# Kernel tuning notes

Measured on AMD Instinct MI355X. Metric: run time of the kernel, lower is better.

The kernel has to match this reference:

```python
import jax, jax.numpy as jnp
import numpy as np

B, I, H, R = 8192, 512, 1024, 64  # batch, input_size, hidden_size, rank (w_rank == u_ranks[-1])


def setup_inputs() -> dict:
    key = jax.random.key(0)
    ks = jax.random.split(key, 11)
    f = jax.random.normal
    return {
        "x": f(ks[0], (B, I), jnp.float32),
        "h": f(ks[1], (B, H), jnp.float32),
        "c": f(ks[2], (B, H), jnp.float32),
        "u_x": 0.1 * f(ks[3], (I, R), jnp.float32),
        "u_h": 0.1 * f(ks[4], (H, R), jnp.float32),
        "v_x": 0.1 * f(ks[5], (4 * H, R), jnp.float32),
        "v_h": 0.1 * f(ks[6], (4 * H, R), jnp.float32),
        "b_x": 0.1 * f(ks[7], (4 * H,), jnp.float32),
        "b_h": 0.1 * f(ks[8], (4 * H,), jnp.float32),
        "dia_x": 0.1 * f(ks[9], (1, I), jnp.float32),
        "dia_h": 0.1 * f(ks[10], (1, H), jnp.float32),
    }


def reference(x, h, c, u_x, u_h, v_x, v_h, b_x, b_h, dia_x, dia_h):
    Bn = x.shape[0]
    # diagonal (vector-multiplication) terms; vm_x padded to hidden size (H >= I)
    vm_x = jnp.pad(dia_x * x, ((0, 0), (0, H - I)))          # [B, H]
    vm_h = dia_h * h                                          # [B, H]
    # low-rank projections: [B,R] @ [R,4H]
    lowered_x = (x @ u_x) @ v_x.T                             # [B, 4H]
    lowered_h = (h @ u_h) @ v_h.T                             # [B, 4H]
    # vectorized form of the 4-gate refinement loop
    v_x4 = v_x.reshape(4, H, R)
    v_h4 = v_h.reshape(4, H, R)
    coef_x = jnp.sum(u_x[None] * v_x4[:, :I, :], axis=-1)    # [4, I]
    coef_h = jnp.sum(u_h[None] * v_h4, axis=-1)              # [4, H]
    ref_x = jnp.pad(x[:, None, :] * coef_x[None], ((0, 0), (0, 0), (0, H - I))).reshape(Bn, 4 * H)
    ref_h = (h[:, None, :] * coef_h[None]).reshape(Bn, 4 * H)
    gx = lowered_x - ref_x + b_x
    gh = lowered_h - ref_h + b_h
    xi, xf, xo, xn = jnp.split(gx, 4, axis=1)
    hi, hf, ho, hn = jnp.split(gh, 4, axis=1)
    z = vm_x + vm_h
    inputgate = jax.nn.sigmoid(xi + hi + z)
    forgetgate = jax.nn.sigmoid(xf + hf + z)
    outputgate = jax.nn.sigmoid(xo + ho + z)
    newgate = jnp.tanh(xn + hn + z)
    c_next = forgetgate * c + inputgate * newgate
    h_next = outputgate * jnp.tanh(c_next)
    return h_next, c_next
```

## Files before the change

### kernel.cpp

```cpp
#include <hip/hip_runtime.h>
#include <hip/hip_bf16.h>

#define B_ 8192
#define I_ 512
#define H_ 1024
#define R_ 64

typedef __bf16 bf16x8 __attribute__((ext_vector_type(8)));
typedef short  s16x8  __attribute__((ext_vector_type(8)));
typedef float  f32x4  __attribute__((ext_vector_type(4)));

static __device__ __forceinline__ short f2bf(float f) {
    union { float f; unsigned u; } v; v.f = f;
    unsigned r = v.u + 0x7fffu + ((v.u >> 16) & 1u);
    return (short)(r >> 16);
}

static __device__ __forceinline__ float sigmoidf_(float v) {
    return 1.f / (1.f + __expf(-v));
}
static __device__ __forceinline__ float tanhf_(float v) {
    return 2.f / (1.f + __expf(-2.f * v)) - 1.f;
}

__global__ __launch_bounds__(256) void prep_kernel(
    const float* __restrict__ u_x, const float* __restrict__ u_h,
    const float* __restrict__ v_x, const float* __restrict__ v_h,
    short* __restrict__ uxT, short* __restrict__ uhT, short* __restrict__ Vc,
    float* __restrict__ coef_x, float* __restrict__ coef_h)
{
    int t = blockIdx.x * 256 + threadIdx.x;
    if (t < 64 * 512) {
        int k = t >> 6, r = t & 63;
        uxT[r * 512 + k] = f2bf(u_x[t]);
        return;
    }
    t -= 64 * 512;
    if (t < 64 * 1024) {
        int k = t >> 6, r = t & 63;
        uhT[r * 1024 + k] = f2bf(u_h[t]);
        return;
    }
    t -= 64 * 1024;
    if (t < 4096 * 128) {
        int n = t >> 7, q = t & 127;
        Vc[t] = f2bf(q < 64 ? v_x[n * 64 + q] : v_h[n * 64 + (q - 64)]);
        return;
    }
    t -= 4096 * 128;
    if (t < 4 * 512) {
        int g = t / 512, j = t % 512;
        const float4* up = (const float4*)(u_x + (size_t)j * 64);
        const float4* vp = (const float4*)(v_x + (size_t)(g * H_ + j) * 64);
        float s = 0.f;
#pragma unroll
        for (int r = 0; r < 16; ++r) {
            float4 a = up[r], b = vp[r];
            s += a.x * b.x + a.y * b.y + a.z * b.z + a.w * b.w;
        }
        coef_x[t] = s;
        return;
    }
    t -= 4 * 512;
    if (t < 4 * 1024) {
        int g = t >> 10, j = t & 1023;
        const float4* up = (const float4*)(u_h + (size_t)j * 64);
        const float4* vp = (const float4*)(v_h + (size_t)(g * H_ + j) * 64);
        float s = 0.f;
#pragma unroll
        for (int r = 0; r < 16; ++r) {
            float4 a = up[r], b = vp[r];
            s += a.x * b.x + a.y * b.y + a.z * b.z + a.w * b.w;
        }
        coef_h[t] = s;
        return;
    }
}

__global__ __launch_bounds__(1024) void stage1_kernel(
    const float* __restrict__ x, const float* __restrict__ h,
    const short* __restrict__ uxT, const short* __restrict__ uhT,
    short* __restrict__ P)
{
    __shared__ short At[64 * 136];
    const int w = threadIdx.x >> 6, lane = threadIdx.x & 63;
    const int quad = lane >> 4, lr = lane & 15;
    const int mt = w >> 2;
    const int n0 = (w & 3) * 16;

    const float* X; const short* UT; int K, co;
    if (blockIdx.y == 0) { X = x; UT = uxT; K = I_; co = 0; }
    else                 { X = h; UT = uhT; K = H_; co = 64; }

    const int b0 = blockIdx.x * 64;
    const int srow = threadIdx.x >> 4;
    const int scol = (threadIdx.x & 15) * 8;

    f32x4 acc = {};
    const short* bp = UT + (size_t)(n0 + lr) * K + quad * 8;
    const short* arow = At + (mt * 16 + lr) * 136 + quad * 8;

    for (int k0 = 0; k0 < K; k0 += 128) {
        const float* src = X + (size_t)(b0 + srow) * K + k0 + scol;
        float4 v0 = ((const float4*)src)[0];
        float4 v1 = ((const float4*)src)[1];
        s16x8 p;
        p[0] = f2bf(v0.x); p[1] = f2bf(v0.y); p[2] = f2bf(v0.z); p[3] = f2bf(v0.w);
        p[4] = f2bf(v1.x); p[5] = f2bf(v1.y); p[6] = f2bf(v1.z); p[7] = f2bf(v1.w);
        __syncthreads();
        *(s16x8*)(At + srow * 136 + scol) = p;
        __syncthreads();
#pragma unroll
        for (int ks = 0; ks < 4; ++ks) {
            bf16x8 bfrag = *(const bf16x8*)(bp + k0 + ks * 32);
            bf16x8 afrag = *(const bf16x8*)(arow + ks * 32);
            acc = __builtin_amdgcn_mfma_f32_16x16x32_bf16(afrag, bfrag, acc, 0, 0, 0);
        }
    }

#pragma unroll
    for (int r = 0; r < 4; ++r)
        P[(size_t)(b0 + mt * 16 + quad * 4 + r) * 128 + co + n0 + lr] = f2bf(acc[r]);
}

__global__ __launch_bounds__(256) void stage2_kernel(
    const short* __restrict__ P, const short* __restrict__ Vc,
    const float* __restrict__ x, const float* __restrict__ h,
    const float* __restrict__ c,
    const float* __restrict__ coef_x, const float* __restrict__ coef_h,
    const float* __restrict__ b_x, const float* __restrict__ b_h,
    const float* __restrict__ dia_x, const float* __restrict__ dia_h,
    float* __restrict__ out)
{
    __shared__ short Bt[4 * 16 * 136];
    const int w = threadIdx.x >> 6, lane = threadIdx.x & 63;
    const int quad = lane >> 4, lr = lane & 15;
    const int b0 = blockIdx.x * 256 + w * 64;
    const int j0 = blockIdx.y * 16;
    const int j = j0 + lr;
    const bool jx = (j < I_);

    {
        const int row = threadIdx.x >> 2;
        const int g = row >> 4, jj = row & 15;
        const int col = (threadIdx.x & 3) * 32;
        const short* src = Vc + (size_t)(g * H_ + j0 + jj) * 128 + col;
        short* dst = Bt + (g * 16 + jj) * 136 + col;
        *(s16x8*)(dst)      = *(const s16x8*)(src);
        *(s16x8*)(dst + 8)  = *(const s16x8*)(src + 8);
        *(s16x8*)(dst + 16) = *(const s16x8*)(src + 16);
        *(s16x8*)(dst + 24) = *(const s16x8*)(src + 24);
    }

    const float dx = jx ? dia_x[j] : 0.f;
    const float dh = dia_h[j];
    float cx[4], ch[4], bsum[4];
#pragma unroll
    for (int g = 0; g < 4; ++g) {
        cx[g]   = jx ? coef_x[g * I_ + j] : 0.f;
        ch[g]   = coef_h[g * H_ + j];
        bsum[g] = b_x[g * H_ + j] + b_h[g * H_ + j];
    }
    __syncthreads();

    for (int mt = 0; mt < 4; ++mt) {
        const int r0 = b0 + mt * 16;

        float xv[4], hv[4], cv[4];
#pragma unroll
        for (int r = 0; r < 4; ++r) {
            const int brow = r0 + quad * 4 + r;
            cv[r] = c[(size_t)brow * H_ + j];
            hv[r] = h[(size_t)brow * H_ + j];
            xv[r] = jx ? x[(size_t)brow * I_ + j] : 0.f;
        }

        f32x4 acc[4] = {};
#pragma unroll
        for (int ks = 0; ks < 4; ++ks) {
            bf16x8 a = *(const bf16x8*)(P + (size_t)(r0 + lr) * 128 + ks * 32 + quad * 8);
#pragma unroll
            for (int g = 0; g < 4; ++g) {
                bf16x8 b = *(const bf16x8*)(Bt + (g * 16 + lr) * 136 + ks * 32 + quad * 8);
                acc[g] = __builtin_amdgcn_mfma_f32_16x16x32_bf16(a, b, acc[g], 0, 0, 0);
            }
        }

#pragma unroll
        for (int r = 0; r < 4; ++r) {
            const int brow = r0 + quad * 4 + r;
            const float xe = xv[r], he = hv[r];
            const float z  = dx * xe + dh * he;

            const float g0 = acc[0][r] - xe * cx[0] - he * ch[0] + bsum[0] + z;
            const float g1 = acc[1][r] - xe * cx[1] - he * ch[1] + bsum[1] + z;
            const float g2 = acc[2][r] - xe * cx[2] - he * ch[2] + bsum[2] + z;
            const float g3 = acc[3][r] - xe * cx[3] - he * ch[3] + bsum[3] + z;

            const float ig = sigmoidf_(g0);
            const float fg = sigmoidf_(g1);
            const float og = sigmoidf_(g2);
            const float ng = tanhf_(g3);

            const float cn = fg * cv[r] + ig * ng;
            const float hn = og * tanhf_(cn);

            out[(size_t)brow * H_ + j] = hn;
            out[(size_t)B_ * H_ + (size_t)brow * H_ + j] = cn;
        }
    }
}

extern "C" void kernel_launch(void* const* d_in, const int* in_sizes, int n_in,
                              void* d_out, int out_size, void* d_ws, size_t ws_size,
                              hipStream_t stream) {
    const float* x     = (const float*)d_in[0];
    const float* h     = (const float*)d_in[1];
    const float* c     = (const float*)d_in[2];
    const float* u_x   = (const float*)d_in[3];
    const float* u_h   = (const float*)d_in[4];
    const float* v_x   = (const float*)d_in[5];
    const float* v_h   = (const float*)d_in[6];
    const float* b_x   = (const float*)d_in[7];
    const float* b_h   = (const float*)d_in[8];
    const float* dia_x = (const float*)d_in[9];
    const float* dia_h = (const float*)d_in[10];
    float* out = (float*)d_out;

    char* ws = (char*)d_ws;
    short* P      = (short*)(ws);
    short* uxT    = (short*)(ws + 2097152);
    short* uhT    = (short*)(ws + 2097152 + 65536);
    short* Vc     = (short*)(ws + 2097152 + 65536 + 131072);
    float* coef_x = (float*)(ws + 2097152 + 65536 + 131072 + 1048576);
    float* coef_h = (float*)(ws + 2097152 + 65536 + 131072 + 1048576 + 8192);

    prep_kernel<<<2456, 256, 0, stream>>>(u_x, u_h, v_x, v_h, uxT, uhT, Vc, coef_x, coef_h);
    stage1_kernel<<<dim3(128, 2), 1024, 0, stream>>>(x, h, uxT, uhT, P);
    stage2_kernel<<<dim3(32, 64), 256, 0, stream>>>(P, Vc, x, h, c,
                                                    coef_x, coef_h, b_x, b_h,
                                                    dia_x, dia_h, out);
}
```

Baseline: 200.6 us.

## Fuse low-rank projection and gate stages into one kernel with LDS-resident P

Merges stage1 and stage2 into a single main_kernel: each block projects 64 batch rows of x and h onto rank space, keeps the bf16 P tile in shared memory, and then computes a 512-wide hidden slice of the gate outputs while prefetching the next column's x/h/c. This removes the global round-trip for P and one launch, and the prep coef computation becomes wave-level shuffle reductions. The trade-off is that the grid shrinks to 256 blocks and each block redoes the projection for both hidden halves, so it does duplicate GEMM work and has less parallelism. V is now read directly from global memory rather than staged in LDS.

```diff
diff --git a/kernel.cpp b/kernel.cpp
--- a/kernel.cpp
+++ b/kernel.cpp
@@ -5,6 +5,7 @@
 #define I_ 512
 #define H_ 1024
 #define R_ 64
+#define PITCH 136
 
 typedef __bf16 bf16x8 __attribute__((ext_vector_type(8)));
 typedef short  s16x8  __attribute__((ext_vector_type(8)));
@@ -15,7 +16,6 @@
     unsigned r = v.u + 0x7fffu + ((v.u >> 16) & 1u);
     return (short)(r >> 16);
 }
-
 static __device__ __forceinline__ float sigmoidf_(float v) {
     return 1.f / (1.f + __expf(-v));
 }
@@ -48,147 +48,157 @@
         return;
     }
     t -= 4096 * 128;
-    if (t < 4 * 512) {
-        int g = t / 512, j = t % 512;
-        const float4* up = (const float4*)(u_x + (size_t)j * 64);
-        const float4* vp = (const float4*)(v_x + (size_t)(g * H_ + j) * 64);
-        float s = 0.f;
-#pragma unroll
-        for (int r = 0; r < 16; ++r) {
-            float4 a = up[r], b = vp[r];
-            s += a.x * b.x + a.y * b.y + a.z * b.z + a.w * b.w;
-        }
-        coef_x[t] = s;
-        return;
-    }
-    t -= 4 * 512;
-    if (t < 4 * 1024) {
-        int g = t >> 10, j = t & 1023;
-        const float4* up = (const float4*)(u_h + (size_t)j * 64);
-        const float4* vp = (const float4*)(v_h + (size_t)(g * H_ + j) * 64);
-        float s = 0.f;
-#pragma unroll
-        for (int r = 0; r < 16; ++r) {
-            float4 a = up[r], b = vp[r];
-            s += a.x * b.x + a.y * b.y + a.z * b.z + a.w * b.w;
-        }
-        coef_h[t] = s;
-        return;
-    }
-}
-
-__global__ __launch_bounds__(1024) void stage1_kernel(
-    const float* __restrict__ x, const float* __restrict__ h,
-    const short* __restrict__ uxT, const short* __restrict__ uhT,
-    short* __restrict__ P)
-{
-    __shared__ short At[64 * 136];
-    const int w = threadIdx.x >> 6, lane = threadIdx.x & 63;
-    const int quad = lane >> 4, lr = lane & 15;
-    const int mt = w >> 2;
-    const int n0 = (w & 3) * 16;
-
-    const float* X; const short* UT; int K, co;
-    if (blockIdx.y == 0) { X = x; UT = uxT; K = I_; co = 0; }
-    else                 { X = h; UT = uhT; K = H_; co = 64; }
-
-    const int b0 = blockIdx.x * 64;
-    const int srow = threadIdx.x >> 4;
-    const int scol = (threadIdx.x & 15) * 8;
-
-    f32x4 acc = {};
-    const short* bp = UT + (size_t)(n0 + lr) * K + quad * 8;
-    const short* arow = At + (mt * 16 + lr) * 136 + quad * 8;
-
-    for (int k0 = 0; k0 < K; k0 += 128) {
-        const float* src = X + (size_t)(b0 + srow) * K + k0 + scol;
-        float4 v0 = ((const float4*)src)[0];
-        float4 v1 = ((const float4*)src)[1];
-        s16x8 p;
-        p[0] = f2bf(v0.x); p[1] = f2bf(v0.y); p[2] = f2bf(v0.z); p[3] = f2bf(v0.w);
-        p[4] = f2bf(v1.x); p[5] = f2bf(v1.y); p[6] = f2bf(v1.z); p[7] = f2bf(v1.w);
-        __syncthreads();
-        *(s16x8*)(At + srow * 136 + scol) = p;
-        __syncthreads();
-#pragma unroll
-        for (int ks = 0; ks < 4; ++ks) {
-            bf16x8 bfrag = *(const bf16x8*)(bp + k0 + ks * 32);
-            bf16x8 afrag = *(const bf16x8*)(arow + ks * 32);
-            acc = __builtin_amdgcn_mfma_f32_16x16x32_bf16(afrag, bfrag, acc, 0, 0, 0);
-        }
-    }
-
-#pragma unroll
-    for (int r = 0; r < 4; ++r)
-        P[(size_t)(b0 + mt * 16 + quad * 4 + r) * 128 + co + n0 + lr] = f2bf(acc[r]);
-}
-
-__global__ __launch_bounds__(256) void stage2_kernel(
-    const short* __restrict__ P, const short* __restrict__ Vc,
+    if (t < 1536 * 64) {
+        const int wid = t >> 6, lane = t & 63;
+        const float* U; const float* V; float* C; int j, JN;
+        if (wid < 512) { U = u_x; V = v_x; C = coef_x; j = wid;       JN = 512;  }
+        else           { U = u_h; V = v_h; C = coef_h; j = wid - 512; JN = 1024; }
+        const float uv = U[(size_t)j * 64 + lane];
+        float s[4];
+#pragma unroll
+        for (int g = 0; g < 4; ++g)
+            s[g] = uv * V[(size_t)(g * H_ + j) * 64 + lane];
+#pragma unroll
+        for (int off = 32; off >= 1; off >>= 1)
+#pragma unroll
+            for (int g = 0; g < 4; ++g)
+                s[g] += __shfl_xor(s[g], off, 64);
+        if (lane == 0)
+#pragma unroll
+            for (int g = 0; g < 4; ++g)
+                C[g * JN + j] = s[g];
+        return;
+    }
+}
+
+__global__ __launch_bounds__(1024, 4) void main_kernel(
     const float* __restrict__ x, const float* __restrict__ h,
     const float* __restrict__ c,
+    const short* __restrict__ uxT, const short* __restrict__ uhT,
+    const short* __restrict__ Vc,
     const float* __restrict__ coef_x, const float* __restrict__ coef_h,
     const float* __restrict__ b_x, const float* __restrict__ b_h,
     const float* __restrict__ dia_x, const float* __restrict__ dia_h,
     float* __restrict__ out)
 {
-    __shared__ short Bt[4 * 16 * 136];
+    __shared__ short At[64 * PITCH];
+    __shared__ short Pl[64 * PITCH];
+
     const int w = threadIdx.x >> 6, lane = threadIdx.x & 63;
     const int quad = lane >> 4, lr = lane & 15;
-    const int b0 = blockIdx.x * 256 + w * 64;
-    const int j0 = blockIdx.y * 16;
-    const int j = j0 + lr;
-    const bool jx = (j < I_);
+    const int mt = w & 3;
+    const int b0 = blockIdx.x * 64;
+
+    const int srow = threadIdx.x >> 4;
+    const int scol = (threadIdx.x & 15) * 8;
 
     {
-        const int row = threadIdx.x >> 2;
-        const int g = row >> 4, jj = row & 15;
-        const int col = (threadIdx.x & 3) * 32;
-        const short* src = Vc + (size_t)(g * H_ + j0 + jj) * 128 + col;
-        short* dst = Bt + (g * 16 + jj) * 136 + col;
-        *(s16x8*)(dst)      = *(const s16x8*)(src);
-        *(s16x8*)(dst + 8)  = *(const s16x8*)(src + 8);
-        *(s16x8*)(dst + 16) = *(const s16x8*)(src + 16);
-        *(s16x8*)(dst + 24) = *(const s16x8*)(src + 24);
-    }
-
-    const float dx = jx ? dia_x[j] : 0.f;
-    const float dh = dia_h[j];
-    float cx[4], ch[4], bsum[4];
-#pragma unroll
-    for (int g = 0; g < 4; ++g) {
-        cx[g]   = jx ? coef_x[g * I_ + j] : 0.f;
-        ch[g]   = coef_h[g * H_ + j];
-        bsum[g] = b_x[g * H_ + j] + b_h[g * H_ + j];
-    }
-    __syncthreads();
-
-    for (int mt = 0; mt < 4; ++mt) {
-        const int r0 = b0 + mt * 16;
-
-        float xv[4], hv[4], cv[4];
+        const int nt = w >> 2;
+        f32x4 accX = {}, accH = {};
+        const short* arow = At + (mt * 16 + lr) * PITCH + quad * 8;
+
+        for (int k0 = 0; k0 < I_; k0 += 128) {
+            const float* src = x + (size_t)(b0 + srow) * I_ + k0 + scol;
+            float4 v0 = ((const float4*)src)[0];
+            float4 v1 = ((const float4*)src)[1];
+            s16x8 p;
+            p[0] = f2bf(v0.x); p[1] = f2bf(v0.y); p[2] = f2bf(v0.z); p[3] = f2bf(v0.w);
+            p[4] = f2bf(v1.x); p[5] = f2bf(v1.y); p[6] = f2bf(v1.z); p[7] = f2bf(v1.w);
+            __syncthreads();
+            *(s16x8*)(At + srow * PITCH + scol) = p;
+            __syncthreads();
+#pragma unroll
+            for (int ks = 0; ks < 4; ++ks) {
+                bf16x8 bfrag = *(const bf16x8*)(uxT + (size_t)(nt * 16 + lr) * I_ + k0 + ks * 32 + quad * 8);
+                bf16x8 afrag = *(const bf16x8*)(arow + ks * 32);
+                accX = __builtin_amdgcn_mfma_f32_16x16x32_bf16(afrag, bfrag, accX, 0, 0, 0);
+            }
+        }
+        for (int k0 = 0; k0 < H_; k0 += 128) {
+            const float* src = h + (size_t)(b0 + srow) * H_ + k0 + scol;
+            float4 v0 = ((const float4*)src)[0];
+            float4 v1 = ((const float4*)src)[1];
+            s16x8 p;
+            p[0] = f2bf(v0.x); p[1] = f2bf(v0.y); p[2] = f2bf(v0.z); p[3] = f2bf(v0.w);
+            p[4] = f2bf(v1.x); p[5] = f2bf(v1.y); p[6] = f2bf(v1.z); p[7] = f2bf(v1.w);
+            __syncthreads();
+            *(s16x8*)(At + srow * PITCH + scol) = p;
+            __syncthreads();
+#pragma unroll
+            for (int ks = 0; ks < 4; ++ks) {
+                bf16x8 bfrag = *(const bf16x8*)(uhT + (size_t)(nt * 16 + lr) * H_ + k0 + ks * 32 + quad * 8);
+                bf16x8 afrag = *(const bf16x8*)(arow + ks * 32);
+                accH = __builtin_amdgcn_mfma_f32_16x16x32_bf16(afrag, bfrag, accH, 0, 0, 0);
+            }
+        }
 #pragma unroll
         for (int r = 0; r < 4; ++r) {
-            const int brow = r0 + quad * 4 + r;
+            short* dst = Pl + (mt * 16 + quad * 4 + r) * PITCH;
+            dst[nt * 16 + lr]      = f2bf(accX[r]);
+            dst[64 + nt * 16 + lr] = f2bf(accH[r]);
+        }
+        __syncthreads();
+    }
+
+    const int jq = w >> 2;
+    int j0 = blockIdx.y * 512 + jq * 128;
+
+    float xv[4], hv[4], cv[4];
+    {
+        const int j = j0 + lr;
+        const bool jx = (j < I_);
+#pragma unroll
+        for (int r = 0; r < 4; ++r) {
+            const int brow = b0 + mt * 16 + quad * 4 + r;
             cv[r] = c[(size_t)brow * H_ + j];
             hv[r] = h[(size_t)brow * H_ + j];
             xv[r] = jx ? x[(size_t)brow * I_ + j] : 0.f;
         }
+    }
+
+    const short* prow = Pl + (mt * 16 + lr) * PITCH;
+
+    for (int tt = 0; tt < 8; ++tt) {
+        const int j = j0 + lr;
+        const bool jx = (j < I_);
+
+        const float dx = jx ? dia_x[j] : 0.f;
+        const float dh = dia_h[j];
+        float cx[4], ch[4], bsum[4];
+#pragma unroll
+        for (int g = 0; g < 4; ++g) {
+            cx[g]   = jx ? coef_x[g * I_ + j] : 0.f;
+            ch[g]   = coef_h[g * H_ + j];
+            bsum[g] = b_x[g * H_ + j] + b_h[g * H_ + j];
+        }
 
         f32x4 acc[4] = {};
 #pragma unroll
         for (int ks = 0; ks < 4; ++ks) {
-            bf16x8 a = *(const bf16x8*)(P + (size_t)(r0 + lr) * 128 + ks * 32 + quad * 8);
+            bf16x8 a = *(const bf16x8*)(prow + ks * 32 + quad * 8);
 #pragma unroll
             for (int g = 0; g < 4; ++g) {
-                bf16x8 b = *(const bf16x8*)(Bt + (g * 16 + lr) * 136 + ks * 32 + quad * 8);
+                bf16x8 b = *(const bf16x8*)(Vc + (size_t)(g * H_ + j0 + lr) * 128 + ks * 32 + quad * 8);
                 acc[g] = __builtin_amdgcn_mfma_f32_16x16x32_bf16(a, b, acc[g], 0, 0, 0);
             }
         }
 
+        float xn[4], hn[4], cn_[4];
+        if (tt < 7) {
+            const int jn = j0 + 16 + lr;
+            const bool jnx = (jn < I_);
+#pragma unroll
+            for (int r = 0; r < 4; ++r) {
+                const int brow = b0 + mt * 16 + quad * 4 + r;
+                cn_[r] = c[(size_t)brow * H_ + jn];
+                hn[r]  = h[(size_t)brow * H_ + jn];
+                xn[r]  = jnx ? x[(size_t)brow * I_ + jn] : 0.f;
+            }
+        }
+
 #pragma unroll
         for (int r = 0; r < 4; ++r) {
-            const int brow = r0 + quad * 4 + r;
+            const int brow = b0 + mt * 16 + quad * 4 + r;
             const float xe = xv[r], he = hv[r];
             const float z  = dx * xe + dh * he;
 
@@ -203,11 +213,15 @@
             const float ng = tanhf_(g3);
 
             const float cn = fg * cv[r] + ig * ng;
-            const float hn = og * tanhf_(cn);
-
-            out[(size_t)brow * H_ + j] = hn;
+            const float hnv = og * tanhf_(cn);
+
+            out[(size_t)brow * H_ + j] = hnv;
             out[(size_t)B_ * H_ + (size_t)brow * H_ + j] = cn;
         }
+
+#pragma unroll
+        for (int r = 0; r < 4; ++r) { xv[r] = xn[r]; hv[r] = hn[r]; cv[r] = cn_[r]; }
+        j0 += 16;
     }
 }
 
@@ -228,16 +242,14 @@
     float* out = (float*)d_out;
 
     char* ws = (char*)d_ws;
-    short* P      = (short*)(ws);
-    short* uxT    = (short*)(ws + 2097152);
-    short* uhT    = (short*)(ws + 2097152 + 65536);
-    short* Vc     = (short*)(ws + 2097152 + 65536 + 131072);
-    float* coef_x = (float*)(ws + 2097152 + 65536 + 131072 + 1048576);
-    float* coef_h = (float*)(ws + 2097152 + 65536 + 131072 + 1048576 + 8192);
-
-    prep_kernel<<<2456, 256, 0, stream>>>(u_x, u_h, v_x, v_h, uxT, uhT, Vc, coef_x, coef_h);
-    stage1_kernel<<<dim3(128, 2), 1024, 0, stream>>>(x, h, uxT, uhT, P);
-    stage2_kernel<<<dim3(32, 64), 256, 0, stream>>>(P, Vc, x, h, c,
-                                                    coef_x, coef_h, b_x, b_h,
-                                                    dia_x, dia_h, out);
-}
+    short* uxT    = (short*)(ws);
+    short* uhT    = (short*)(ws + 65536);
+    short* Vc     = (short*)(ws + 65536 + 131072);
+    float* coef_x = (float*)(ws + 65536 + 131072 + 1048576);
+    float* coef_h = (float*)(ws + 65536 + 131072 + 1048576 + 8192);
+
+    prep_kernel<<<2816, 256, 0, stream>>>(u_x, u_h, v_x, v_h, uxT, uhT, Vc, coef_x, coef_h);
+    main_kernel<<<dim3(128, 2), 1024, 0, stream>>>(x, h, c, uxT, uhT, Vc,
+                                                   coef_x, coef_h, b_x, b_h,
+                                                   dia_x, dia_h, out);
+}
```

Result: slower. 234.5 us (+16.9%).

## Prefetch next tiles in stage kernels, shrink blocks, and warp-reduce coefficients

Applied to the files above, without the earlier changes.

Stage1 now uses 256-thread blocks covering 16 batch rows and register-prefetches the next K chunk of x/h while the MFMAs run. Stage2 drops the shared-memory staging of Vc and reads B fragments straight from global/L2, uses single-wave blocks, and software-pipelines the loads of P, c, h and x for the next 16-row tile. The coefficient dot products in prep are recomputed with one wave per column plus shuffle reductions instead of a serial per-thread loop. These changes aim to hide global load latency and raise occupancy, at the cost of redundant Vc reads from L2 across blocks and higher register pressure.

```diff
diff --git a/kernel.cpp b/kernel.cpp
--- a/kernel.cpp
+++ b/kernel.cpp
@@ -15,7 +15,6 @@
     unsigned r = v.u + 0x7fffu + ((v.u >> 16) & 1u);
     return (short)(r >> 16);
 }
-
 static __device__ __forceinline__ float sigmoidf_(float v) {
     return 1.f / (1.f + __expf(-v));
 }
@@ -48,68 +47,66 @@
         return;
     }
     t -= 4096 * 128;
-    if (t < 4 * 512) {
-        int g = t / 512, j = t % 512;
-        const float4* up = (const float4*)(u_x + (size_t)j * 64);
-        const float4* vp = (const float4*)(v_x + (size_t)(g * H_ + j) * 64);
-        float s = 0.f;
-#pragma unroll
-        for (int r = 0; r < 16; ++r) {
-            float4 a = up[r], b = vp[r];
-            s += a.x * b.x + a.y * b.y + a.z * b.z + a.w * b.w;
-        }
-        coef_x[t] = s;
-        return;
-    }
-    t -= 4 * 512;
-    if (t < 4 * 1024) {
-        int g = t >> 10, j = t & 1023;
-        const float4* up = (const float4*)(u_h + (size_t)j * 64);
-        const float4* vp = (const float4*)(v_h + (size_t)(g * H_ + j) * 64);
-        float s = 0.f;
-#pragma unroll
-        for (int r = 0; r < 16; ++r) {
-            float4 a = up[r], b = vp[r];
-            s += a.x * b.x + a.y * b.y + a.z * b.z + a.w * b.w;
-        }
-        coef_h[t] = s;
-        return;
-    }
-}
-
-__global__ __launch_bounds__(1024) void stage1_kernel(
+    if (t < 1536 * 64) {
+        const int wid = t >> 6, lane = t & 63;
+        const float* U; const float* V; float* C; int j, JN;
+        if (wid < 512) { U = u_x; V = v_x; C = coef_x; j = wid;       JN = 512;  }
+        else           { U = u_h; V = v_h; C = coef_h; j = wid - 512; JN = 1024; }
+        const float uv = U[(size_t)j * 64 + lane];
+        float s[4];
+#pragma unroll
+        for (int g = 0; g < 4; ++g)
+            s[g] = uv * V[(size_t)(g * H_ + j) * 64 + lane];
+#pragma unroll
+        for (int off = 32; off >= 1; off >>= 1)
+#pragma unroll
+            for (int g = 0; g < 4; ++g)
+                s[g] += __shfl_xor(s[g], off, 64);
+        if (lane == 0)
+#pragma unroll
+            for (int g = 0; g < 4; ++g)
+                C[g * JN + j] = s[g];
+        return;
+    }
+}
+
+__global__ __launch_bounds__(256) void stage1_kernel(
     const float* __restrict__ x, const float* __restrict__ h,
     const short* __restrict__ uxT, const short* __restrict__ uhT,
     short* __restrict__ P)
 {
-    __shared__ short At[64 * 136];
+    __shared__ short At[16 * 136];
     const int w = threadIdx.x >> 6, lane = threadIdx.x & 63;
     const int quad = lane >> 4, lr = lane & 15;
-    const int mt = w >> 2;
-    const int n0 = (w & 3) * 16;
+    const int n0 = w * 16;
 
     const float* X; const short* UT; int K, co;
     if (blockIdx.y == 0) { X = x; UT = uxT; K = I_; co = 0; }
     else                 { X = h; UT = uhT; K = H_; co = 64; }
 
-    const int b0 = blockIdx.x * 64;
+    const int b0 = blockIdx.x * 16;
     const int srow = threadIdx.x >> 4;
     const int scol = (threadIdx.x & 15) * 8;
 
     f32x4 acc = {};
     const short* bp = UT + (size_t)(n0 + lr) * K + quad * 8;
-    const short* arow = At + (mt * 16 + lr) * 136 + quad * 8;
+    const short* arow = At + lr * 136 + quad * 8;
+    const float* srcbase = X + (size_t)(b0 + srow) * K + scol;
+
+    float4 c0 = ((const float4*)(srcbase))[0];
+    float4 c1 = ((const float4*)(srcbase))[1];
 
     for (int k0 = 0; k0 < K; k0 += 128) {
-        const float* src = X + (size_t)(b0 + srow) * K + k0 + scol;
-        float4 v0 = ((const float4*)src)[0];
-        float4 v1 = ((const float4*)src)[1];
         s16x8 p;
-        p[0] = f2bf(v0.x); p[1] = f2bf(v0.y); p[2] = f2bf(v0.z); p[3] = f2bf(v0.w);
-        p[4] = f2bf(v1.x); p[5] = f2bf(v1.y); p[6] = f2bf(v1.z); p[7] = f2bf(v1.w);
+        p[0] = f2bf(c0.x); p[1] = f2bf(c0.y); p[2] = f2bf(c0.z); p[3] = f2bf(c0.w);
+        p[4] = f2bf(c1.x); p[5] = f2bf(c1.y); p[6] = f2bf(c1.z); p[7] = f2bf(c1.w);
         __syncthreads();
         *(s16x8*)(At + srow * 136 + scol) = p;
         __syncthreads();
+        if (k0 + 128 < K) {
+            c0 = ((const float4*)(srcbase + k0 + 128))[0];
+            c1 = ((const float4*)(srcbase + k0 + 128))[1];
+        }
 #pragma unroll
         for (int ks = 0; ks < 4; ++ks) {
             bf16x8 bfrag = *(const bf16x8*)(bp + k0 + ks * 32);
@@ -120,10 +117,10 @@
 
 #pragma unroll
     for (int r = 0; r < 4; ++r)
-        P[(size_t)(b0 + mt * 16 + quad * 4 + r) * 128 + co + n0 + lr] = f2bf(acc[r]);
-}
-
-__global__ __launch_bounds__(256) void stage2_kernel(
+        P[(size_t)(b0 + quad * 4 + r) * 128 + co + n0 + lr] = f2bf(acc[r]);
+}
+
+__global__ __launch_bounds__(64) void stage2_kernel(
     const short* __restrict__ P, const short* __restrict__ Vc,
     const float* __restrict__ x, const float* __restrict__ h,
     const float* __restrict__ c,
@@ -132,25 +129,12 @@
     const float* __restrict__ dia_x, const float* __restrict__ dia_h,
     float* __restrict__ out)
 {
-    __shared__ short Bt[4 * 16 * 136];
-    const int w = threadIdx.x >> 6, lane = threadIdx.x & 63;
+    const int lane = threadIdx.x;
     const int quad = lane >> 4, lr = lane & 15;
-    const int b0 = blockIdx.x * 256 + w * 64;
+    const int b0 = blockIdx.x * 64;
     const int j0 = blockIdx.y * 16;
     const int j = j0 + lr;
     const bool jx = (j < I_);
-
-    {
-        const int row = threadIdx.x >> 2;
-        const int g = row >> 4, jj = row & 15;
-        const int col = (threadIdx.x & 3) * 32;
-        const short* src = Vc + (size_t)(g * H_ + j0 + jj) * 128 + col;
-        short* dst = Bt + (g * 16 + jj) * 136 + col;
-        *(s16x8*)(dst)      = *(const s16x8*)(src);
-        *(s16x8*)(dst + 8)  = *(const s16x8*)(src + 8);
-        *(s16x8*)(dst + 16) = *(const s16x8*)(src + 16);
-        *(s16x8*)(dst + 24) = *(const s16x8*)(src + 24);
-    }
 
     const float dx = jx ? dia_x[j] : 0.f;
     const float dh = dia_h[j];
@@ -161,34 +145,51 @@
         ch[g]   = coef_h[g * H_ + j];
         bsum[g] = b_x[g * H_ + j] + b_h[g * H_ + j];
     }
-    __syncthreads();
-
+
+    bf16x8 a[4];
+#pragma unroll
+    for (int ks = 0; ks < 4; ++ks)
+        a[ks] = *(const bf16x8*)(P + (size_t)(b0 + lr) * 128 + ks * 32 + quad * 8);
+    float xv[4], hv[4], cv[4];
+#pragma unroll
+    for (int r = 0; r < 4; ++r) {
+        const int brow = b0 + quad * 4 + r;
+        cv[r] = c[(size_t)brow * H_ + j];
+        hv[r] = h[(size_t)brow * H_ + j];
+        xv[r] = jx ? x[(size_t)brow * I_ + j] : 0.f;
+    }
+
+#pragma unroll
     for (int mt = 0; mt < 4; ++mt) {
-        const int r0 = b0 + mt * 16;
-
-        float xv[4], hv[4], cv[4];
+        bf16x8 an[4];
+        float xn[4], hn[4], cn2[4];
+        if (mt < 3) {
+            const int rb = b0 + (mt + 1) * 16;
+#pragma unroll
+            for (int ks = 0; ks < 4; ++ks)
+                an[ks] = *(const bf16x8*)(P + (size_t)(rb + lr) * 128 + ks * 32 + quad * 8);
+#pragma unroll
+            for (int r = 0; r < 4; ++r) {
+                const int brow = rb + quad * 4 + r;
+                cn2[r] = c[(size_t)brow * H_ + j];
+                hn[r]  = h[(size_t)brow * H_ + j];
+                xn[r]  = jx ? x[(size_t)brow * I_ + j] : 0.f;
+            }
+        }
+
+        f32x4 acc[4] = {};
+#pragma unroll
+        for (int ks = 0; ks < 4; ++ks) {
+#pragma unroll
+            for (int g = 0; g < 4; ++g) {
+                bf16x8 b = *(const bf16x8*)(Vc + (size_t)(g * H_ + j0 + lr) * 128 + ks * 32 + quad * 8);
+                acc[g] = __builtin_amdgcn_mfma_f32_16x16x32_bf16(a[ks], b, acc[g], 0, 0, 0);
+            }
+        }
+
 #pragma unroll
         for (int r = 0; r < 4; ++r) {
-            const int brow = r0 + quad * 4 + r;
-            cv[r] = c[(size_t)brow * H_ + j];
-            hv[r] = h[(size_t)brow * H_ + j];
-            xv[r] = jx ? x[(size_t)brow * I_ + j] : 0.f;
-        }
-
-        f32x4 acc[4] = {};
-#pragma unroll
-        for (int ks = 0; ks < 4; ++ks) {
-            bf16x8 a = *(const bf16x8*)(P + (size_t)(r0 + lr) * 128 + ks * 32 + quad * 8);
-#pragma unroll
-            for (int g = 0; g < 4; ++g) {
-                bf16x8 b = *(const bf16x8*)(Bt + (g * 16 + lr) * 136 + ks * 32 + quad * 8);
-                acc[g] = __builtin_amdgcn_mfma_f32_16x16x32_bf16(a, b, acc[g], 0, 0, 0);
-            }
-        }
-
-#pragma unroll
-        for (int r = 0; r < 4; ++r) {
-            const int brow = r0 + quad * 4 + r;
+            const int brow = b0 + mt * 16 + quad * 4 + r;
             const float xe = xv[r], he = hv[r];
             const float z  = dx * xe + dh * he;
 
@@ -203,10 +204,17 @@
             const float ng = tanhf_(g3);
 
             const float cn = fg * cv[r] + ig * ng;
-            const float hn = og * tanhf_(cn);
-
-            out[(size_t)brow * H_ + j] = hn;
+            const float hnv = og * tanhf_(cn);
+
+            out[(size_t)brow * H_ + j] = hnv;
             out[(size_t)B_ * H_ + (size_t)brow * H_ + j] = cn;
+        }
+
+        if (mt < 3) {
+#pragma unroll
+            for (int ks = 0; ks < 4; ++ks) a[ks] = an[ks];
+#pragma unroll
+            for (int r = 0; r < 4; ++r) { xv[r] = xn[r]; hv[r] = hn[r]; cv[r] = cn2[r]; }
         }
     }
 }
@@ -235,9 +243,9 @@
     float* coef_x = (float*)(ws + 2097152 + 65536 + 131072 + 1048576);
     float* coef_h = (float*)(ws + 2097152 + 65536 + 131072 + 1048576 + 8192);
 
-    prep_kernel<<<2456, 256, 0, stream>>>(u_x, u_h, v_x, v_h, uxT, uhT, Vc, coef_x, coef_h);
-    stage1_kernel<<<dim3(128, 2), 1024, 0, stream>>>(x, h, uxT, uhT, P);
-    stage2_kernel<<<dim3(32, 64), 256, 0, stream>>>(P, Vc, x, h, c,
+    prep_kernel<<<2816, 256, 0, stream>>>(u_x, u_h, v_x, v_h, uxT, uhT, Vc, coef_x, coef_h);
+    stage1_kernel<<<dim3(512, 2), 256, 0, stream>>>(x, h, uxT, uhT, P);
+    stage2_kernel<<<dim3(128, 64), 64, 0, stream>>>(P, Vc, x, h, c,
                                                     coef_x, coef_h, b_x, b_h,
                                                     dia_x, dia_h, out);
 }
```

Measured after the change: 229.6 us. 14.4% more time.
